# Kernel tuning notes

Measured on AMD Instinct MI355X. Metric: run time of the kernel, lower is better.

The kernel has to match this reference:

```python
import jax, jax.numpy as jnp
import numpy as np

T, B, NIN, N, A = 100, 32, 512, 2048, 2
DT = 1e-3
THR = 1.0
ALPHA = float(np.exp(-DT / 0.01))


def setup_inputs() -> dict:
    key = jax.random.key(0)
    k1, k2, k3, k4 = jax.random.split(key, 4)
    rates = jax.random.uniform(k1, (T, B, NIN), dtype=jnp.float32) * 100.0  # Hz
    noise = jax.random.uniform(k2, (T, B, NIN), dtype=jnp.float32)  # Poisson thresholds
    Win = jax.random.normal(k3, (A, NIN, N), dtype=jnp.float32) * (1.5 / np.sqrt(NIN))
    Wrec = jax.random.normal(k4, (A, A, N, N), dtype=jnp.float32) * (1.0 / np.sqrt(N))
    return {"rates": rates, "noise": noise, "Win": Win, "Wrec": Wrec}


def reference(rates, noise, Win, Wrec):
    dtype = rates.dtype
    V0 = jnp.zeros((A, B, N), dtype)   # membrane potentials, all areas
    Xd0 = jnp.zeros((A, B, N), dtype)  # delayed cross-area spikes (reset())

    def step(carry, inp):
        V, Xd = carry
        rate_t, noise_t = inp
        # PoissonInput: Bernoulli spikes with prob rate*dt
        Xi = (noise_t < rate_t * DT).astype(dtype)  # [B, NIN]
        # per-area input current: feedforward + all-to-all cross-area recurrent
        I = jnp.einsum('bi,ain->abn', Xi, Win) + jnp.einsum('sbn,sanm->abm', Xd, Wrec)
        # LIF: leak, reset on previous spike, integrate
        V_new = ALPHA * V * (1.0 - Xd) + I
        S = (V_new >= THR).astype(dtype)  # [A, B, N]
        return (V_new, S), (Xi, S)

    (_, _), (Xis, Ss) = jax.lax.scan(step, (V0, Xd0), (rates, noise))
    # Xis: [T, B, NIN]; Ss: [T, A, B, N] -> per-area stacked outputs
    return (Xis, Ss[:, 0], Ss[:, 1])
```

## Files before the change

### kernel.cpp

```cpp
#include <hip/hip_runtime.h>

#define T_STEPS 100
#define BATCH   32
#define NIN     512
#define NN      2048
#define AREAS   2

#define ALPHA_D 0.9048374180359595

__global__ __launch_bounds__(256)
void k0_xi(const float* __restrict__ rates, const float* __restrict__ noise,
           float* __restrict__ outXi, unsigned* __restrict__ xi_mask)
{
    int el = blockIdx.x * 256 + threadIdx.x;
    float r = rates[el], nz = noise[el];
    float p = __fmul_rn(r, 0.001f);
    int spike = (nz < p) ? 1 : 0;
    outXi[el] = (float)spike;
    if (spike) {
        int t = el >> 14;
        int b = (el >> 9) & 31;
        int i = el & (NIN - 1);
        atomicOr(&xi_mask[(t * 32 + b) * 16 + (i >> 5)], 1u << (i & 31));
    }
}

__global__ __launch_bounds__(256)
void k_ff(const float* __restrict__ Win, const unsigned* __restrict__ xi_mask,
          float* __restrict__ Iff)
{
    const int tb  = blockIdx.x;
    const int a   = blockIdx.y;
    const int tid = threadIdx.x;

    __shared__ unsigned mws[16];
    if (tid < 16) mws[tid] = xi_mask[tb * 16 + tid];
    __syncthreads();

    const float* Wa = Win + ((size_t)a << 20) + (tid << 3);
    float4 A0 = {0,0,0,0}, A1 = {0,0,0,0};
    for (int w = 0; w < 16; ++w) {
        unsigned mw = mws[w];
        int base_i = w << 5;
        while (mw) {
            int i = base_i + (__ffs(mw) - 1);
            mw &= mw - 1;
            const float* rp = Wa + ((size_t)i << 11);
            float4 w0 = ((const float4*)rp)[0];
            float4 w1 = ((const float4*)rp)[1];
            A0.x += w0.x; A0.y += w0.y; A0.z += w0.z; A0.w += w0.w;
            A1.x += w1.x; A1.y += w1.y; A1.z += w1.z; A1.w += w1.w;
        }
    }
    float* op = Iff + (((size_t)tb * 2 + a) << 11) + (tid << 3);
    ((float4*)op)[0] = A0;
    ((float4*)op)[1] = A1;
}

#define OFF_OF(rr) ((((rr) >> 11) << 23) + (((rr) & 2047) << 11))

#define GLDS(src, dst) __builtin_amdgcn_global_load_lds(                      \
    (const __attribute__((address_space(1))) void*)(src),                     \
    (__attribute__((address_space(3))) void*)(dst), 16, 0, 0)

__global__ __launch_bounds__(256, 2)
void k_steps(const float* __restrict__ Wrec,
             unsigned long long* __restrict__ smask,
             const float* __restrict__ Iff,
             float* __restrict__ outS)
{
    const int tid = threadIdx.x;
    const int bx  = blockIdx.x;
    const int s   = bx & 15;
    const int b   = bx >> 4;
    const int a   = s >> 3;
    const int m0  = (s & 7) << 8;
    const int c   = m0 + tid;
    const int wv  = tid >> 6;
    const int lane = tid & 63;

    __shared__ __align__(16) float stage[64 * 256];
    __shared__ unsigned mws[128];
    __shared__ __align__(16) unsigned short lrec[AREAS * NN];
    __shared__ int base[128];
    __shared__ int cnt_rec;
    __shared__ unsigned nsp[8];

    const float* __restrict__ Wb = Wrec + ((size_t)a << 22) + m0 + (lane << 2);
    const int rr_self = (a << 11) | c;
    const int wsel = rr_self >> 5;
    const int w0   = s << 3;

    float vst = 0.0f;

    for (int t = 0; t < T_STEPS; ++t) {
        unsigned long long* cur = smask + (size_t)(t & 1) * (BATCH * 128) + (b << 7);
        unsigned long long* nxt = smask + (size_t)((t + 1) & 1) * (BATCH * 128) + (b << 7);

        if (tid < 128) {
            unsigned long long v = __hip_atomic_load(&cur[tid], __ATOMIC_RELAXED,
                                                     __HIP_MEMORY_SCOPE_AGENT);
            while ((unsigned)(v >> 32) != (unsigned)t) {
                __builtin_amdgcn_s_sleep(4);
                v = __hip_atomic_load(&cur[tid], __ATOMIC_RELAXED,
                                      __HIP_MEMORY_SCOPE_AGENT);
            }
            mws[tid] = (unsigned)v;
        }
        if (tid < 8) nsp[tid] = 0u;
        float accf = Iff[((((size_t)t * BATCH + b) * 2 + a) << 11) + c];
        __syncthreads();

        if (tid < 64) {
            int c0 = __popc(mws[2 * tid]), c1 = __popc(mws[2 * tid + 1]);
            int cc = c0 + c1, incl = cc;
            #pragma unroll
            for (int d = 1; d < 64; d <<= 1) {
                int v = __shfl_up(incl, d, 64);
                if (tid >= d) incl += v;
            }
            base[2 * tid]     = incl - cc;
            base[2 * tid + 1] = incl - c1;
            if (tid == 63) cnt_rec = incl;
        }
        __syncthreads();

        if (tid < 128) {
            unsigned w = mws[tid];
            if (w) {
                int off = base[tid];
                int bb = tid << 5;
                while (w) {
                    int p = __ffs(w) - 1;
                    lrec[off++] = (unsigned short)(bb + p);
                    w &= w - 1;
                }
            }
        }
        __syncthreads();

        const int nrec = cnt_rec;
        unsigned xd = (mws[wsel] >> (tid & 31)) & 1u;

        float accr = 0.0f;
        for (int j = 0; j < nrec; j += 64) {
            const int cnt = min(64, nrec - j);
            for (int k = wv; k < cnt; k += 4) {
                int row = lrec[j + k];
                GLDS(Wb + OFF_OF(row), &stage[k << 8]);
            }
            asm volatile("s_waitcnt vmcnt(0)" ::: "memory");
            __builtin_amdgcn_sched_barrier(0);
            __syncthreads();
            int k = 0;
            for (; k + 4 <= cnt; k += 4) {
                float w0v = stage[((k + 0) << 8) + tid];
                float w1v = stage[((k + 1) << 8) + tid];
                float w2v = stage[((k + 2) << 8) + tid];
                float w3v = stage[((k + 3) << 8) + tid];
                accr = __fadd_rn(accr, w0v);
                accr = __fadd_rn(accr, w1v);
                accr = __fadd_rn(accr, w2v);
                accr = __fadd_rn(accr, w3v);
            }
            for (; k < cnt; ++k)
                accr = __fadd_rn(accr, stage[(k << 8) + tid]);
            __syncthreads();
        }

        float I  = __fadd_rn(accf, accr);
        float v  = __fmul_rn((float)ALPHA_D, vst);
        if (xd) v = 0.0f;
        float vn = __fadd_rn(v, I);
        vst = vn;
        int S = (vn >= 1.0f) ? 1 : 0;
        if (S) atomicOr(&nsp[tid >> 5], 1u << (tid & 31));
        __syncthreads();

        if (t < T_STEPS - 1 && tid < 8) {
            unsigned long long pv =
                ((unsigned long long)(unsigned)(t + 1) << 32) | nsp[tid];
            atomicExch(&nxt[w0 + tid], pv);
        }
        outS[(size_t)a * (T_STEPS * BATCH * NN)
             + (((size_t)t * BATCH + b) << 11) + c] = (float)S;
    }
}
#undef OFF_OF
#undef GLDS

extern "C" void kernel_launch(void* const* d_in, const int* in_sizes, int n_in,
                              void* d_out, int out_size, void* d_ws, size_t ws_size,
                              hipStream_t stream)
{
    const float* rates = (const float*)d_in[0];
    const float* noise = (const float*)d_in[1];
    const float* Win   = (const float*)d_in[2];
    const float* Wrec  = (const float*)d_in[3];
    float* out = (float*)d_out;

    char* ws = (char*)d_ws;
    unsigned* xi_mask = (unsigned*)ws;
    unsigned long long* smask = (unsigned long long*)(ws + 204800);
    float* Iff = (float*)(ws + 270336);

    hipMemsetAsync(d_ws, 0, 270336, stream);

    k0_xi<<<6400, 256, 0, stream>>>(rates, noise, out, xi_mask);
    k_ff<<<dim3(3200, 2), 256, 0, stream>>>(Win, xi_mask, Iff);

    float* outS = out + (size_t)T_STEPS * BATCH * NIN;
    void* args[] = { (void*)&Wrec, (void*)&smask, (void*)&Iff, (void*)&outS };
    hipLaunchCooperativeKernel((const void*)k_steps, dim3(512), dim3(256),
                               args, 0, stream);
}
```

Before: 1.090 ms.

## Double-buffer recurrent weight row staging and remap block-to-batch assignment

Replaces the single 64-row staging pass with 32-row rounds split across two LDS halves. The next round's global-to-LDS loads are issued before the current round is summed, with a partial vmcnt wait so load latency overlaps the accumulation. It also remaps block indices so that blocks sharing a weight slice (same area/column segment) are spread differently across the grid, and shortens the spin-wait sleep to cut polling latency. Risks: using raw s_barrier without memory fences relies on the waitcnt for LDS visibility, and faster polling adds memory traffic.

```diff
diff --git a/kernel.cpp b/kernel.cpp
--- a/kernel.cpp
+++ b/kernel.cpp
@@ -71,8 +71,8 @@
 {
     const int tid = threadIdx.x;
     const int bx  = blockIdx.x;
-    const int s   = bx & 15;
-    const int b   = bx >> 4;
+    const int s   = (bx & 7) | (((bx >> 8) & 1) << 3);
+    const int b   = (bx >> 3) & 31;
     const int a   = s >> 3;
     const int m0  = (s & 7) << 8;
     const int c   = m0 + tid;
@@ -101,7 +101,7 @@
             unsigned long long v = __hip_atomic_load(&cur[tid], __ATOMIC_RELAXED,
                                                      __HIP_MEMORY_SCOPE_AGENT);
             while ((unsigned)(v >> 32) != (unsigned)t) {
-                __builtin_amdgcn_s_sleep(4);
+                __builtin_amdgcn_s_sleep(1);
                 v = __hip_atomic_load(&cur[tid], __ATOMIC_RELAXED,
                                       __HIP_MEMORY_SCOPE_AGENT);
             }
@@ -142,31 +142,48 @@
         const int nrec = cnt_rec;
         unsigned xd = (mws[wsel] >> (tid & 31)) & 1u;
 
+#define ISSUE_ROUND(r, h) do {                                                \
+            const unsigned short* lp_ = &lrec[(r) << 5];                      \
+            for (int k_ = wv; k_ < 32; k_ += 4)                               \
+                GLDS(Wb + OFF_OF((int)lp_[k_]),                               \
+                     &stage[((h) << 13) + (k_ << 8)]);                        \
+        } while (0)
+
         float accr = 0.0f;
-        for (int j = 0; j < nrec; j += 64) {
-            const int cnt = min(64, nrec - j);
-            for (int k = wv; k < cnt; k += 4) {
-                int row = lrec[j + k];
-                GLDS(Wb + OFF_OF(row), &stage[k << 8]);
-            }
+        const int nfull = nrec >> 5;
+        const int rem   = nrec & 31;
+        if (nfull > 0) {
+            ISSUE_ROUND(0, 0);
+            for (int r = 0; r < nfull; ++r) {
+                const int h = r & 1;
+                if (r + 1 < nfull) {
+                    ISSUE_ROUND(r + 1, h ^ 1);
+                    asm volatile("s_waitcnt vmcnt(8)" ::: "memory");
+                } else {
+                    asm volatile("s_waitcnt vmcnt(0)" ::: "memory");
+                }
+                __builtin_amdgcn_sched_barrier(0);
+                __builtin_amdgcn_s_barrier();
+                const float* cb = &stage[h << 13];
+                #pragma unroll 4
+                for (int k = 0; k < 32; ++k)
+                    accr = __fadd_rn(accr, cb[(k << 8) + tid]);
+                __builtin_amdgcn_s_barrier();
+            }
+        }
+        if (rem) {
+            const int h = nfull & 1;
+            const unsigned short* lp = &lrec[nfull << 5];
+            for (int k = wv; k < rem; k += 4)
+                GLDS(Wb + OFF_OF((int)lp[k]), &stage[(h << 13) + (k << 8)]);
             asm volatile("s_waitcnt vmcnt(0)" ::: "memory");
             __builtin_amdgcn_sched_barrier(0);
-            __syncthreads();
-            int k = 0;
-            for (; k + 4 <= cnt; k += 4) {
-                float w0v = stage[((k + 0) << 8) + tid];
-                float w1v = stage[((k + 1) << 8) + tid];
-                float w2v = stage[((k + 2) << 8) + tid];
-                float w3v = stage[((k + 3) << 8) + tid];
-                accr = __fadd_rn(accr, w0v);
-                accr = __fadd_rn(accr, w1v);
-                accr = __fadd_rn(accr, w2v);
-                accr = __fadd_rn(accr, w3v);
-            }
-            for (; k < cnt; ++k)
-                accr = __fadd_rn(accr, stage[(k << 8) + tid]);
-            __syncthreads();
-        }
+            __builtin_amdgcn_s_barrier();
+            const float* cb = &stage[h << 13];
+            for (int k = 0; k < rem; ++k)
+                accr = __fadd_rn(accr, cb[(k << 8) + tid]);
+        }
+#undef ISSUE_ROUND
 
         float I  = __fadd_rn(accf, accr);
         float v  = __fmul_rn((float)ALPHA_D, vst);
```

Measured after the change: 1.173 ms. 7.6% more time.

## Triple-buffer recurrent weight row staging to overlap loads with accumulation

Applied to the files above, without the earlier changes.

Replaces the load-all-then-sum batches of up to 64 rows with a three-slot ring of 20-row rounds. Rounds are issued ahead and consumed under partial vmcnt waits, so global-to-LDS loads overlap the summation. The spike list is padded with zero indices so every wave always issues five loads per round, which keeps the fixed vmcnt counts valid. In exchange it adds more barriers per step and some wasted padding loads, and it uses a smaller LDS stage buffer.

```diff
diff --git a/kernel.cpp b/kernel.cpp
--- a/kernel.cpp
+++ b/kernel.cpp
@@ -79,9 +79,9 @@
     const int wv  = tid >> 6;
     const int lane = tid & 63;
 
-    __shared__ __align__(16) float stage[64 * 256];
+    __shared__ __align__(16) float stage[3 * 20 * 256];
     __shared__ unsigned mws[128];
-    __shared__ __align__(16) unsigned short lrec[AREAS * NN];
+    __shared__ __align__(16) unsigned short lrec[4128];
     __shared__ int base[128];
     __shared__ int cnt_rec;
     __shared__ unsigned nsp[8];
@@ -136,37 +136,57 @@
                     w &= w - 1;
                 }
             }
+        } else if (tid < 160) {
+            lrec[cnt_rec + (tid - 128)] = 0;
         }
         __syncthreads();
 
         const int nrec = cnt_rec;
         unsigned xd = (mws[wsel] >> (tid & 31)) & 1u;
 
+#define ISSUE_ROUND(r) do {                                                   \
+            const unsigned short* lp_ = &lrec[(r) * 20];                      \
+            const int bo_ = ((r) % 3) * 5120;                                 \
+            GLDS(Wb + OFF_OF((int)lp_[wv]),      &stage[bo_ + (wv << 8)]);    \
+            GLDS(Wb + OFF_OF((int)lp_[wv + 4]),  &stage[bo_ + ((wv + 4) << 8)]);  \
+            GLDS(Wb + OFF_OF((int)lp_[wv + 8]),  &stage[bo_ + ((wv + 8) << 8)]);  \
+            GLDS(Wb + OFF_OF((int)lp_[wv + 12]), &stage[bo_ + ((wv + 12) << 8)]); \
+            GLDS(Wb + OFF_OF((int)lp_[wv + 16]), &stage[bo_ + ((wv + 16) << 8)]); \
+        } while (0)
+
         float accr = 0.0f;
-        for (int j = 0; j < nrec; j += 64) {
-            const int cnt = min(64, nrec - j);
-            for (int k = wv; k < cnt; k += 4) {
-                int row = lrec[j + k];
-                GLDS(Wb + OFF_OF(row), &stage[k << 8]);
-            }
-            asm volatile("s_waitcnt vmcnt(0)" ::: "memory");
-            __builtin_amdgcn_sched_barrier(0);
-            __syncthreads();
-            int k = 0;
-            for (; k + 4 <= cnt; k += 4) {
-                float w0v = stage[((k + 0) << 8) + tid];
-                float w1v = stage[((k + 1) << 8) + tid];
-                float w2v = stage[((k + 2) << 8) + tid];
-                float w3v = stage[((k + 3) << 8) + tid];
-                accr = __fadd_rn(accr, w0v);
-                accr = __fadd_rn(accr, w1v);
-                accr = __fadd_rn(accr, w2v);
-                accr = __fadd_rn(accr, w3v);
-            }
-            for (; k < cnt; ++k)
-                accr = __fadd_rn(accr, stage[(k << 8) + tid]);
-            __syncthreads();
-        }
+        if (nrec > 0) {
+            const int nrounds = (nrec + 19) / 20;
+            if (nrounds > 0) ISSUE_ROUND(0);
+            if (nrounds > 1) ISSUE_ROUND(1);
+            if (nrounds > 2) ISSUE_ROUND(2);
+            for (int r = 0; r < nrounds; ++r) {
+                const int ahead = nrounds - 1 - r;
+                if (ahead >= 2)      asm volatile("s_waitcnt vmcnt(10)" ::: "memory");
+                else if (ahead == 1) asm volatile("s_waitcnt vmcnt(5)"  ::: "memory");
+                else                 asm volatile("s_waitcnt vmcnt(0)"  ::: "memory");
+                __builtin_amdgcn_sched_barrier(0);
+                __builtin_amdgcn_s_barrier();
+                const float* cb = &stage[(r % 3) * 5120];
+                int lim = nrec - r * 20; if (lim > 20) lim = 20;
+                int k = 0;
+                for (; k + 4 <= lim; k += 4) {
+                    float q0 = cb[((k + 0) << 8) + tid];
+                    float q1 = cb[((k + 1) << 8) + tid];
+                    float q2 = cb[((k + 2) << 8) + tid];
+                    float q3 = cb[((k + 3) << 8) + tid];
+                    accr = __fadd_rn(accr, q0);
+                    accr = __fadd_rn(accr, q1);
+                    accr = __fadd_rn(accr, q2);
+                    accr = __fadd_rn(accr, q3);
+                }
+                for (; k < lim; ++k)
+                    accr = __fadd_rn(accr, cb[(k << 8) + tid]);
+                __builtin_amdgcn_s_barrier();
+                if (r + 3 < nrounds) ISSUE_ROUND(r + 3);
+            }
+        }
+#undef ISSUE_ROUND
 
         float I  = __fadd_rn(accf, accr);
         float v  = __fmul_rn((float)ALPHA_D, vst);
```

Result: slower. 1.235 ms (+13.4%).
